# Kernel optimization log

Measured on AMD Instinct MI355X. Metric: run time of the kernel, lower is better.

## Reference

```python
import jax, jax.numpy as jnp
import numpy as np
from jax import lax

B, T = 64, 2048
ENC, DEC, ATT = 512, 1024, 128
NFILT, KSIZE = 32, 31
PAD = KSIZE // 2


def setup_inputs() -> dict:
    key = jax.random.key(0)
    ks = jax.random.split(key, 9)
    query = jax.random.normal(ks[0], (B, 1, DEC), dtype=jnp.float32)
    keys = jax.random.normal(ks[1], (B, T, ENC), dtype=jnp.float32)
    prev_weights = jax.random.uniform(ks[2], (B, T), dtype=jnp.float32)
    mask = jax.random.randint(ks[3], (B, T), 0, 2, dtype=jnp.int32)
    # params stored as [in, out] (transpose of torch Linear weight); same math
    W1 = jax.random.normal(ks[4], (ENC, ATT), dtype=jnp.float32) * (ENC ** -0.5)
    W2 = jax.random.normal(ks[5], (DEC, ATT), dtype=jnp.float32) * (DEC ** -0.5)
    V = jax.random.normal(ks[6], (ATT,), dtype=jnp.float32) * (ATT ** -0.5)
    conv_w = jax.random.normal(ks[7], (NFILT, 1, KSIZE), dtype=jnp.float32) * (KSIZE ** -0.5)
    loc_dense = jax.random.normal(ks[8], (NFILT, ATT), dtype=jnp.float32) * (NFILT ** -0.5)
    return {"query": query, "keys": keys, "prev_weights": prev_weights, "mask": mask,
            "W1": W1, "W2": W2, "V": V, "conv_w": conv_w, "loc_dense": loc_dense}


def reference(query, keys, prev_weights, mask, W1, W2, V, conv_w, loc_dense):
    proj_key = jnp.einsum('bte,ea->bta', keys, W1)          # [B,T,A]
    proj_query = jnp.einsum('bqd,da->bqa', query, W2)       # [B,1,A]
    # location conv: input [B,1,T], kernel [F,1,K], 'same' padding -> [B,F,T]
    loc_feat = lax.conv_general_dilated(prev_weights[:, None, :], conv_w,
                                        window_strides=(1,), padding=[(PAD, PAD)],
                                        dimension_numbers=('NCH', 'OIH', 'NCH'))
    proj_loc = jnp.einsum('bft,fa->bta', loc_feat, loc_dense)  # [B,T,A]
    scores = jnp.einsum('bta,a->bt', jnp.tanh(proj_key + proj_query + proj_loc), V)
    scores = jnp.where(mask == 0, -1e9, scores)
    weights = jax.nn.softmax(scores, axis=-1)                # [B,T]
    context = jnp.einsum('bt,bte->be', weights, keys)[:, None, :]  # [B,1,ENC]
    return context, weights
```

## Files before the change

kernel.cpp:

```cpp
#include <hip/hip_runtime.h>

typedef __attribute__((ext_vector_type(4))) float f32x4;
typedef __attribute__((ext_vector_type(8))) short bf16x8;

#define T_LEN 2048
#define ENC   512
#define DEC   1024
#define ATT   128
#define NB    64
#define NTB   64
#define NSTEP 17

__device__ __forceinline__ unsigned short f2bf_rne(float x) {
  unsigned int u = __builtin_bit_cast(unsigned int, x);
  u += 0x7fff + ((u >> 16) & 1);
  return (unsigned short)(u >> 16);
}
__device__ __forceinline__ short f2bf_fast(float x) {
  unsigned int u = __builtin_bit_cast(unsigned int, x);
  return (short)((u + 0x8000u) >> 16);
}

__device__ __forceinline__ float fast_tanh(float x) {
  float e = __expf(2.f * x);
  return 1.f - 2.f / (e + 1.f);
}

__global__ __launch_bounds__(128) void prep(
    const float* __restrict__ query, const float* __restrict__ W2,
    const float* __restrict__ W1, const float* __restrict__ convw,
    const float* __restrict__ ldense,
    float* __restrict__ pq, unsigned short* __restrict__ Bl) {
  int bidx = blockIdx.x;
  if (bidx < NB) {
    int a = threadIdx.x;
    const float* q = query + bidx * DEC;
    float a0 = 0.f, a1 = 0.f, a2 = 0.f, a3 = 0.f;
    for (int d = 0; d < DEC; d += 4) {
      a0 += q[d]     * W2[(d)     * ATT + a];
      a1 += q[d + 1] * W2[(d + 1) * ATT + a];
      a2 += q[d + 2] * W2[(d + 2) * ATT + a];
      a3 += q[d + 3] * W2[(d + 3) * ATT + a];
    }
    pq[bidx * ATT + a] = (a0 + a1) + (a2 + a3);
  } else {
    int a = bidx - NB;
    int n = a >> 4, rs = a & 15;
    for (int k = threadIdx.x; k < NSTEP * 32; k += 128) {
      float v = 0.f;
      if (k < 512) {
        v = W1[k * ATT + a];
      } else if (k < 543) {
        int kc = k - 512;
        #pragma unroll
        for (int f = 0; f < 32; ++f) v += convw[f * 31 + kc] * ldense[f * ATT + a];
      }
      int t = k >> 5, g = (k & 31) >> 3, j = k & 7;
      Bl[(((t * 8 + n) * 64 + g * 16 + rs) << 3) + j] = f2bf_rne(v);
    }
  }
}

__global__ __launch_bounds__(64, 2) void lsa_main(
    const float* __restrict__ keys, const float* __restrict__ prev,
    const int* __restrict__ mask, const unsigned short* __restrict__ Bl,
    const float* __restrict__ pq, const float* __restrict__ Vv,
    float* __restrict__ wout, float* __restrict__ dpart, float* __restrict__ cpart) {
  __shared__ float e_vals[32];

  const int lane = threadIdx.x;
  const int bid = blockIdx.x;
  const int b = bid >> 6;
  const int row0 = (bid & 63) * 32;
  const int rsel = lane & 15, grp = lane >> 4;

  const float* keyrow = keys + ((size_t)b * T_LEN + row0 + rsel) * ENC + grp * 8;
  const unsigned short* Bp = Bl + lane * 8;

  f32x4 acc[2][8];
  #pragma unroll
  for (int m = 0; m < 2; ++m)
    #pragma unroll
    for (int n = 0; n < 8; ++n) acc[m][n] = (f32x4)0.f;

  f32x4 A0, A1, A2, A3, B0, B1, B2, B3, C0, C1, C2, C3;
  bf16x8 P0, P1, P2, P3, P4, P5, P6, P7;
  bf16x8 Q0, Q1, Q2, Q3, Q4, Q5, Q6, Q7;

#define SB() __builtin_amdgcn_sched_barrier(0)

#define LOADK(S, t_) do { \
    S##0 = *(const f32x4*)(keyrow + (t_) * 32); \
    S##1 = *(const f32x4*)(keyrow + (t_) * 32 + 4); \
    S##2 = *(const f32x4*)(keyrow + 16 * ENC + (t_) * 32); \
    S##3 = *(const f32x4*)(keyrow + 16 * ENC + (t_) * 32 + 4); } while (0)

#define LOADP(S) do { \
    _Pragma("unroll") \
    for (int j_ = 0; j_ < 4; ++j_) { \
      int kk0 = grp * 8 + j_, kk1 = grp * 8 + 4 + j_; \
      int p00 = row0 + rsel + kk0 - 15, p01 = row0 + rsel + kk1 - 15; \
      S##0[j_] = (kk0 < 31 && p00 >= 0 && p00 < T_LEN) ? prev[b * T_LEN + p00] : 0.f; \
      S##1[j_] = (kk1 < 31 && p01 >= 0 && p01 < T_LEN) ? prev[b * T_LEN + p01] : 0.f; \
      S##2[j_] = (kk0 < 31 && p00 + 16 >= 0 && p00 + 16 < T_LEN) ? prev[b * T_LEN + p00 + 16] : 0.f; \
      S##3[j_] = (kk1 < 31 && p01 + 16 >= 0 && p01 + 16 < T_LEN) ? prev[b * T_LEN + p01 + 16] : 0.f; \
    } } while (0)

#define LOADB(S, t_) do { \
    S##0 = *(const bf16x8*)(Bp + ((t_) * 8 + 0) * 512); \
    S##1 = *(const bf16x8*)(Bp + ((t_) * 8 + 1) * 512); \
    S##2 = *(const bf16x8*)(Bp + ((t_) * 8 + 2) * 512); \
    S##3 = *(const bf16x8*)(Bp + ((t_) * 8 + 3) * 512); \
    S##4 = *(const bf16x8*)(Bp + ((t_) * 8 + 4) * 512); \
    S##5 = *(const bf16x8*)(Bp + ((t_) * 8 + 5) * 512); \
    S##6 = *(const bf16x8*)(Bp + ((t_) * 8 + 6) * 512); \
    S##7 = *(const bf16x8*)(Bp + ((t_) * 8 + 7) * 512); } while (0)

#define STEP(S, BB) do { \
    bf16x8 af0, af1; \
    _Pragma("unroll") \
    for (int j_ = 0; j_ < 4; ++j_) { \
      af0[j_] = f2bf_fast(S##0[j_]); af0[4 + j_] = f2bf_fast(S##1[j_]); \
      af1[j_] = f2bf_fast(S##2[j_]); af1[4 + j_] = f2bf_fast(S##3[j_]); \
    } \
    acc[0][0] = __builtin_amdgcn_mfma_f32_16x16x32_bf16(af0, BB##0, acc[0][0], 0, 0, 0); \
    acc[1][0] = __builtin_amdgcn_mfma_f32_16x16x32_bf16(af1, BB##0, acc[1][0], 0, 0, 0); \
    acc[0][1] = __builtin_amdgcn_mfma_f32_16x16x32_bf16(af0, BB##1, acc[0][1], 0, 0, 0); \
    acc[1][1] = __builtin_amdgcn_mfma_f32_16x16x32_bf16(af1, BB##1, acc[1][1], 0, 0, 0); \
    acc[0][2] = __builtin_amdgcn_mfma_f32_16x16x32_bf16(af0, BB##2, acc[0][2], 0, 0, 0); \
    acc[1][2] = __builtin_amdgcn_mfma_f32_16x16x32_bf16(af1, BB##2, acc[1][2], 0, 0, 0); \
    acc[0][3] = __builtin_amdgcn_mfma_f32_16x16x32_bf16(af0, BB##3, acc[0][3], 0, 0, 0); \
    acc[1][3] = __builtin_amdgcn_mfma_f32_16x16x32_bf16(af1, BB##3, acc[1][3], 0, 0, 0); \
    acc[0][4] = __builtin_amdgcn_mfma_f32_16x16x32_bf16(af0, BB##4, acc[0][4], 0, 0, 0); \
    acc[1][4] = __builtin_amdgcn_mfma_f32_16x16x32_bf16(af1, BB##4, acc[1][4], 0, 0, 0); \
    acc[0][5] = __builtin_amdgcn_mfma_f32_16x16x32_bf16(af0, BB##5, acc[0][5], 0, 0, 0); \
    acc[1][5] = __builtin_amdgcn_mfma_f32_16x16x32_bf16(af1, BB##5, acc[1][5], 0, 0, 0); \
    acc[0][6] = __builtin_amdgcn_mfma_f32_16x16x32_bf16(af0, BB##6, acc[0][6], 0, 0, 0); \
    acc[1][6] = __builtin_amdgcn_mfma_f32_16x16x32_bf16(af1, BB##6, acc[1][6], 0, 0, 0); \
    acc[0][7] = __builtin_amdgcn_mfma_f32_16x16x32_bf16(af0, BB##7, acc[0][7], 0, 0, 0); \
    acc[1][7] = __builtin_amdgcn_mfma_f32_16x16x32_bf16(af1, BB##7, acc[1][7], 0, 0, 0); } while (0)

  LOADK(A, 0); LOADK(B, 1); LOADB(P, 0);
  LOADK(C, 2);  LOADB(Q, 1);  SB(); STEP(A, P);
  LOADK(A, 3);  LOADB(P, 2);  SB(); STEP(B, Q);
  LOADK(B, 4);  LOADB(Q, 3);  SB(); STEP(C, P);
  LOADK(C, 5);  LOADB(P, 4);  SB(); STEP(A, Q);
  LOADK(A, 6);  LOADB(Q, 5);  SB(); STEP(B, P);
  LOADK(B, 7);  LOADB(P, 6);  SB(); STEP(C, Q);
  LOADK(C, 8);  LOADB(Q, 7);  SB(); STEP(A, P);
  LOADK(A, 9);  LOADB(P, 8);  SB(); STEP(B, Q);
  LOADK(B, 10); LOADB(Q, 9);  SB(); STEP(C, P);
  LOADK(C, 11); LOADB(P, 10); SB(); STEP(A, Q);
  LOADK(A, 12); LOADB(Q, 11); SB(); STEP(B, P);
  LOADK(B, 13); LOADB(P, 12); SB(); STEP(C, Q);
  LOADK(C, 14); LOADB(Q, 13); SB(); STEP(A, P);
  LOADK(A, 15); LOADB(P, 14); SB(); STEP(B, Q);
  LOADP(B);     LOADB(Q, 15); SB(); STEP(C, P);
  LOADB(P, 16); SB(); STEP(A, Q);
  STEP(B, P);

  float psum[2][4];
  #pragma unroll
  for (int m = 0; m < 2; ++m)
    #pragma unroll
    for (int i = 0; i < 4; ++i) psum[m][i] = 0.f;
  #pragma unroll
  for (int n = 0; n < 8; ++n) {
    int c = n * 16 + rsel;
    float pqv = pq[b * ATT + c];
    float vv = Vv[c];
    #pragma unroll
    for (int m = 0; m < 2; ++m)
      #pragma unroll
      for (int i = 0; i < 4; ++i)
        psum[m][i] += vv * fast_tanh(acc[m][n][i] + pqv);
  }
  #pragma unroll
  for (int m = 0; m < 2; ++m)
    #pragma unroll
    for (int i = 0; i < 4; ++i) {
      float v = psum[m][i];
      v += __shfl_xor(v, 1, 64);
      v += __shfl_xor(v, 2, 64);
      v += __shfl_xor(v, 4, 64);
      v += __shfl_xor(v, 8, 64);
      psum[m][i] = v;
    }
  float esum = 0.f;
  if (rsel == 0) {
    #pragma unroll
    for (int m = 0; m < 2; ++m)
      #pragma unroll
      for (int i = 0; i < 4; ++i) {
        int r = m * 16 + grp * 4 + i;
        int gr = b * T_LEN + row0 + r;
        float e = (mask[gr] == 0) ? 0.f : __expf(psum[m][i]);
        wout[gr] = e;
        e_vals[r] = e;
        esum += e;
      }
  }
  esum += __shfl_xor(esum, 16, 64);
  esum += __shfl_xor(esum, 32, 64);
  if (lane == 0) dpart[bid] = esum;
  __syncthreads();

  {
    const float* kb = keys + ((size_t)b * T_LEN + row0) * ENC + lane * 8;
    f32x4 c0 = (f32x4)0.f, c1 = (f32x4)0.f;
    #pragma unroll
    for (int r = 0; r < 32; ++r) {
      float e = e_vals[r];
      f32x4 k0 = *(const f32x4*)(kb + (size_t)r * ENC);
      f32x4 k1 = *(const f32x4*)(kb + (size_t)r * ENC + 4);
      c0 += e * k0;
      c1 += e * k1;
    }
    *(f32x4*)(cpart + (size_t)bid * ENC + lane * 8) = c0;
    *(f32x4*)(cpart + (size_t)bid * ENC + lane * 8 + 4) = c1;
  }
}

__global__ __launch_bounds__(256) void lsa_finalize(
    const float* __restrict__ dpart, const float* __restrict__ cpart,
    float* __restrict__ out) {
  int b = blockIdx.x, tid = threadIdx.x;
  float d = 0.f;
  #pragma unroll
  for (int i = 0; i < NTB; ++i) d += dpart[b * NTB + i];
  float inv = 1.f / d;
  for (int e = tid; e < ENC; e += 256) {
    float c = 0.f;
    #pragma unroll
    for (int i = 0; i < NTB; ++i) c += cpart[((size_t)(b * NTB + i)) * ENC + e];
    out[b * ENC + e] = c * inv;
  }
  float* wrow = out + NB * ENC + (size_t)b * T_LEN;
  for (int t = tid; t < T_LEN; t += 256) wrow[t] *= inv;
}

extern "C" void kernel_launch(void* const* d_in, const int* in_sizes, int n_in,
                              void* d_out, int out_size, void* d_ws, size_t ws_size,
                              hipStream_t stream) {
  const float* query  = (const float*)d_in[0];
  const float* keys   = (const float*)d_in[1];
  const float* prev   = (const float*)d_in[2];
  const int*   mask   = (const int*)d_in[3];
  const float* W1     = (const float*)d_in[4];
  const float* W2     = (const float*)d_in[5];
  const float* V      = (const float*)d_in[6];
  const float* convw  = (const float*)d_in[7];
  const float* ldense = (const float*)d_in[8];
  float* out = (float*)d_out;

  char* ws = (char*)d_ws;
  unsigned short* Bl = (unsigned short*)ws;
  float* pq    = (float*)(ws + 139264);
  float* dpart = (float*)(ws + 139264 + 32768);
  float* cpart = (float*)(ws + 139264 + 32768 + 16384);

  prep<<<dim3(192), dim3(128), 0, stream>>>(query, W2, W1, convw, ldense, pq, Bl);
  lsa_main<<<dim3(NB * NTB), dim3(64), 0, stream>>>(keys, prev, mask, Bl, pq, V,
                                                    out + NB * ENC, dpart, cpart);
  lsa_finalize<<<dim3(NB), dim3(256), 0, stream>>>(dpart, cpart, out);
}
```

Before: 137.7 us.

## Stage keys and weights through LDS with async global-to-LDS copies

Replaces the direct register loads of key rows and bf16 weight fragments with asynchronous global_load_lds copies into a triple-buffered key area and double-buffered weight area in shared memory. Key rows are laid out with an XOR swizzle to avoid bank conflicts, and explicit vmcnt waits drive the pipeline. Each step then reads its MFMA operands from LDS. This frees vector registers and drops the two-waves-per-SIMD launch bound, but it uses about 37 KB of LDS per 64-thread block, which may limit occupancy, and adds LDS read traffic and hand-tuned wait counts that must stay correct.

After: 136.5 us. Within noise of the previous version (-0.9%).

```diff
diff --git a/kernel.cpp b/kernel.cpp
--- a/kernel.cpp
+++ b/kernel.cpp
@@ -11,6 +11,14 @@
 #define NTB   64
 #define NSTEP 17
 
+typedef unsigned int u32;
+typedef __attribute__((address_space(1))) const u32 gu32;
+typedef __attribute__((address_space(3))) u32 lu32;
+
+__device__ __forceinline__ void async_copy16(const void* g, void* l) {
+  __builtin_amdgcn_global_load_lds((gu32*)g, (lu32*)l, 16, 0, 0);
+}
+
 __device__ __forceinline__ unsigned short f2bf_rne(float x) {
   unsigned int u = __builtin_bit_cast(unsigned int, x);
   u += 0x7fff + ((u >> 16) & 1);
@@ -20,7 +28,6 @@
   unsigned int u = __builtin_bit_cast(unsigned int, x);
   return (short)((u + 0x8000u) >> 16);
 }
-
 __device__ __forceinline__ float fast_tanh(float x) {
   float e = __expf(2.f * x);
   return 1.f - 2.f / (e + 1.f);
@@ -61,21 +68,26 @@
   }
 }
 
-__global__ __launch_bounds__(64, 2) void lsa_main(
+__global__ __launch_bounds__(64) void lsa_main(
     const float* __restrict__ keys, const float* __restrict__ prev,
     const int* __restrict__ mask, const unsigned short* __restrict__ Bl,
     const float* __restrict__ pq, const float* __restrict__ Vv,
     float* __restrict__ wout, float* __restrict__ dpart, float* __restrict__ cpart) {
-  __shared__ float e_vals[32];
+  __shared__ f32x4 SHv[2312];
+  char* SHc = (char*)SHv;
 
   const int lane = threadIdx.x;
   const int bid = blockIdx.x;
   const int b = bid >> 6;
   const int row0 = (bid & 63) * 32;
   const int rsel = lane & 15, grp = lane >> 4;
-
-  const float* keyrow = keys + ((size_t)b * T_LEN + row0 + rsel) * ENC + grp * 8;
-  const unsigned short* Bp = Bl + lane * 8;
+  const int lr = lane >> 3, cp = lane & 7;
+  const int gc = cp ^ lr;
+  const int ca0 = (2 * grp) ^ (rsel & 7);
+  const int ca1 = ca0 ^ 1;
+
+  const float* gAsrc = keys + ((size_t)b * T_LEN + row0 + lr) * ENC + gc * 4;
+  const unsigned short* Bsrc = Bl + lane * 8;
 
   f32x4 acc[2][8];
   #pragma unroll
@@ -83,82 +95,110 @@
     #pragma unroll
     for (int n = 0; n < 8; ++n) acc[m][n] = (f32x4)0.f;
 
-  f32x4 A0, A1, A2, A3, B0, B1, B2, B3, C0, C1, C2, C3;
-  bf16x8 P0, P1, P2, P3, P4, P5, P6, P7;
-  bf16x8 Q0, Q1, Q2, Q3, Q4, Q5, Q6, Q7;
-
-#define SB() __builtin_amdgcn_sched_barrier(0)
-
-#define LOADK(S, t_) do { \
-    S##0 = *(const f32x4*)(keyrow + (t_) * 32); \
-    S##1 = *(const f32x4*)(keyrow + (t_) * 32 + 4); \
-    S##2 = *(const f32x4*)(keyrow + 16 * ENC + (t_) * 32); \
-    S##3 = *(const f32x4*)(keyrow + 16 * ENC + (t_) * 32 + 4); } while (0)
-
-#define LOADP(S) do { \
+#define WAITVM_(n) asm volatile("s_waitcnt vmcnt(" #n ")" ::: "memory")
+#define WAITVM(n) WAITVM_(n)
+#define LGKM0 asm volatile("s_waitcnt lgkmcnt(0)" ::: "memory")
+
+#define STAGE_A(t_, buf_) do { \
+    const float* s_ = gAsrc + (t_) * 32; \
+    char* d_ = SHc + (buf_) * 4096; \
+    async_copy16(s_,            d_); \
+    async_copy16(s_ +  8 * ENC, d_ + 1024); \
+    async_copy16(s_ + 16 * ENC, d_ + 2048); \
+    async_copy16(s_ + 24 * ENC, d_ + 3072); } while (0)
+
+#define STAGE_B(t_, buf_) do { \
+    const unsigned short* s_ = Bsrc + (size_t)(t_) * 4096; \
+    char* d_ = SHc + 12288 + (buf_) * 8192; \
+    _Pragma("unroll") \
+    for (int n_ = 0; n_ < 8; ++n_) \
+      async_copy16(s_ + n_ * 512, d_ + n_ * 1024); } while (0)
+
+#define STAGE_B16() do { \
+    const unsigned short* s_ = Bsrc + (size_t)16 * 4096; \
+    char* d_ = SHc + 28672; \
+    _Pragma("unroll") \
+    for (int n_ = 0; n_ < 8; ++n_) \
+      async_copy16(s_ + n_ * 512, d_ + n_ * 1024); } while (0)
+
+#define KSTEP(ab_, bb_, STAGECODE) do { \
+    const char* Ab_ = SHc + (ab_) * 4096; \
+    const char* Bb_ = SHc + 12288 + (bb_) * 8192; \
+    f32x4 x00 = *(const f32x4*)(Ab_ + rsel * 128 + ca0 * 16); \
+    f32x4 x01 = *(const f32x4*)(Ab_ + rsel * 128 + ca1 * 16); \
+    f32x4 x10 = *(const f32x4*)(Ab_ + (16 + rsel) * 128 + ca0 * 16); \
+    f32x4 x11 = *(const f32x4*)(Ab_ + (16 + rsel) * 128 + ca1 * 16); \
+    bf16x8 bfr[8]; \
+    _Pragma("unroll") \
+    for (int n_ = 0; n_ < 8; ++n_) \
+      bfr[n_] = *(const bf16x8*)(Bb_ + n_ * 1024 + lane * 16); \
+    LGKM0; \
+    STAGECODE; \
+    bf16x8 af0, af1; \
     _Pragma("unroll") \
     for (int j_ = 0; j_ < 4; ++j_) { \
-      int kk0 = grp * 8 + j_, kk1 = grp * 8 + 4 + j_; \
-      int p00 = row0 + rsel + kk0 - 15, p01 = row0 + rsel + kk1 - 15; \
-      S##0[j_] = (kk0 < 31 && p00 >= 0 && p00 < T_LEN) ? prev[b * T_LEN + p00] : 0.f; \
-      S##1[j_] = (kk1 < 31 && p01 >= 0 && p01 < T_LEN) ? prev[b * T_LEN + p01] : 0.f; \
-      S##2[j_] = (kk0 < 31 && p00 + 16 >= 0 && p00 + 16 < T_LEN) ? prev[b * T_LEN + p00 + 16] : 0.f; \
-      S##3[j_] = (kk1 < 31 && p01 + 16 >= 0 && p01 + 16 < T_LEN) ? prev[b * T_LEN + p01 + 16] : 0.f; \
+      af0[j_] = f2bf_fast(x00[j_]); af0[4 + j_] = f2bf_fast(x01[j_]); \
+      af1[j_] = f2bf_fast(x10[j_]); af1[4 + j_] = f2bf_fast(x11[j_]); \
+    } \
+    _Pragma("unroll") \
+    for (int n_ = 0; n_ < 8; ++n_) { \
+      acc[0][n_] = __builtin_amdgcn_mfma_f32_16x16x32_bf16(af0, bfr[n_], acc[0][n_], 0, 0, 0); \
+      acc[1][n_] = __builtin_amdgcn_mfma_f32_16x16x32_bf16(af1, bfr[n_], acc[1][n_], 0, 0, 0); \
     } } while (0)
 
-#define LOADB(S, t_) do { \
-    S##0 = *(const bf16x8*)(Bp + ((t_) * 8 + 0) * 512); \
-    S##1 = *(const bf16x8*)(Bp + ((t_) * 8 + 1) * 512); \
-    S##2 = *(const bf16x8*)(Bp + ((t_) * 8 + 2) * 512); \
-    S##3 = *(const bf16x8*)(Bp + ((t_) * 8 + 3) * 512); \
-    S##4 = *(const bf16x8*)(Bp + ((t_) * 8 + 4) * 512); \
-    S##5 = *(const bf16x8*)(Bp + ((t_) * 8 + 5) * 512); \
-    S##6 = *(const bf16x8*)(Bp + ((t_) * 8 + 6) * 512); \
-    S##7 = *(const bf16x8*)(Bp + ((t_) * 8 + 7) * 512); } while (0)
-
-#define STEP(S, BB) do { \
-    bf16x8 af0, af1; \
-    _Pragma("unroll") \
-    for (int j_ = 0; j_ < 4; ++j_) { \
-      af0[j_] = f2bf_fast(S##0[j_]); af0[4 + j_] = f2bf_fast(S##1[j_]); \
-      af1[j_] = f2bf_fast(S##2[j_]); af1[4 + j_] = f2bf_fast(S##3[j_]); \
-    } \
-    acc[0][0] = __builtin_amdgcn_mfma_f32_16x16x32_bf16(af0, BB##0, acc[0][0], 0, 0, 0); \
-    acc[1][0] = __builtin_amdgcn_mfma_f32_16x16x32_bf16(af1, BB##0, acc[1][0], 0, 0, 0); \
-    acc[0][1] = __builtin_amdgcn_mfma_f32_16x16x32_bf16(af0, BB##1, acc[0][1], 0, 0, 0); \
-    acc[1][1] = __builtin_amdgcn_mfma_f32_16x16x32_bf16(af1, BB##1, acc[1][1], 0, 0, 0); \
-    acc[0][2] = __builtin_amdgcn_mfma_f32_16x16x32_bf16(af0, BB##2, acc[0][2], 0, 0, 0); \
-    acc[1][2] = __builtin_amdgcn_mfma_f32_16x16x32_bf16(af1, BB##2, acc[1][2], 0, 0, 0); \
-    acc[0][3] = __builtin_amdgcn_mfma_f32_16x16x32_bf16(af0, BB##3, acc[0][3], 0, 0, 0); \
-    acc[1][3] = __builtin_amdgcn_mfma_f32_16x16x32_bf16(af1, BB##3, acc[1][3], 0, 0, 0); \
-    acc[0][4] = __builtin_amdgcn_mfma_f32_16x16x32_bf16(af0, BB##4, acc[0][4], 0, 0, 0); \
-    acc[1][4] = __builtin_amdgcn_mfma_f32_16x16x32_bf16(af1, BB##4, acc[1][4], 0, 0, 0); \
-    acc[0][5] = __builtin_amdgcn_mfma_f32_16x16x32_bf16(af0, BB##5, acc[0][5], 0, 0, 0); \
-    acc[1][5] = __builtin_amdgcn_mfma_f32_16x16x32_bf16(af1, BB##5, acc[1][5], 0, 0, 0); \
-    acc[0][6] = __builtin_amdgcn_mfma_f32_16x16x32_bf16(af0, BB##6, acc[0][6], 0, 0, 0); \
-    acc[1][6] = __builtin_amdgcn_mfma_f32_16x16x32_bf16(af1, BB##6, acc[1][6], 0, 0, 0); \
-    acc[0][7] = __builtin_amdgcn_mfma_f32_16x16x32_bf16(af0, BB##7, acc[0][7], 0, 0, 0); \
-    acc[1][7] = __builtin_amdgcn_mfma_f32_16x16x32_bf16(af1, BB##7, acc[1][7], 0, 0, 0); } while (0)
-
-  LOADK(A, 0); LOADK(B, 1); LOADB(P, 0);
-  LOADK(C, 2);  LOADB(Q, 1);  SB(); STEP(A, P);
-  LOADK(A, 3);  LOADB(P, 2);  SB(); STEP(B, Q);
-  LOADK(B, 4);  LOADB(Q, 3);  SB(); STEP(C, P);
-  LOADK(C, 5);  LOADB(P, 4);  SB(); STEP(A, Q);
-  LOADK(A, 6);  LOADB(Q, 5);  SB(); STEP(B, P);
-  LOADK(B, 7);  LOADB(P, 6);  SB(); STEP(C, Q);
-  LOADK(C, 8);  LOADB(Q, 7);  SB(); STEP(A, P);
-  LOADK(A, 9);  LOADB(P, 8);  SB(); STEP(B, Q);
-  LOADK(B, 10); LOADB(Q, 9);  SB(); STEP(C, P);
-  LOADK(C, 11); LOADB(P, 10); SB(); STEP(A, Q);
-  LOADK(A, 12); LOADB(Q, 11); SB(); STEP(B, P);
-  LOADK(B, 13); LOADB(P, 12); SB(); STEP(C, Q);
-  LOADK(C, 14); LOADB(Q, 13); SB(); STEP(A, P);
-  LOADK(A, 15); LOADB(P, 14); SB(); STEP(B, Q);
-  LOADP(B);     LOADB(Q, 15); SB(); STEP(C, P);
-  LOADB(P, 16); SB(); STEP(A, Q);
-  STEP(B, P);
-
+  f32x4 CV0, CV1, CV2, CV3;
+  #pragma unroll
+  for (int j = 0; j < 4; ++j) {
+    int kk0 = grp * 8 + j, kk1 = grp * 8 + 4 + j;
+    int p00 = row0 + rsel + kk0 - 15, p01 = row0 + rsel + kk1 - 15;
+    CV0[j] = (kk0 < 31 && p00 >= 0 && p00 < T_LEN) ? prev[b * T_LEN + p00] : 0.f;
+    CV1[j] = (kk1 < 31 && p01 >= 0 && p01 < T_LEN) ? prev[b * T_LEN + p01] : 0.f;
+    CV2[j] = (kk0 < 31 && p00 + 16 >= 0 && p00 + 16 < T_LEN) ? prev[b * T_LEN + p00 + 16] : 0.f;
+    CV3[j] = (kk1 < 31 && p01 + 16 >= 0 && p01 + 16 < T_LEN) ? prev[b * T_LEN + p01 + 16] : 0.f;
+  }
+
+  STAGE_B(0, 0); STAGE_A(0, 0);
+  STAGE_B(1, 1); STAGE_A(1, 1);
+  STAGE_A(2, 2);
+
+  WAITVM(16); KSTEP(0, 0, { STAGE_B(2, 0);  STAGE_A(3, 0);  });
+  WAITVM(16); KSTEP(1, 1, { STAGE_B(3, 1);  STAGE_A(4, 1);  });
+  WAITVM(16); KSTEP(2, 0, { STAGE_B(4, 0);  STAGE_A(5, 2);  });
+  WAITVM(16); KSTEP(0, 1, { STAGE_B(5, 1);  STAGE_A(6, 0);  });
+  WAITVM(16); KSTEP(1, 0, { STAGE_B(6, 0);  STAGE_A(7, 1);  });
+  WAITVM(16); KSTEP(2, 1, { STAGE_B(7, 1);  STAGE_A(8, 2);  });
+  WAITVM(16); KSTEP(0, 0, { STAGE_B(8, 0);  STAGE_A(9, 0);  });
+  WAITVM(16); KSTEP(1, 1, { STAGE_B(9, 1);  STAGE_A(10, 1); });
+  WAITVM(16); KSTEP(2, 0, { STAGE_B(10, 0); STAGE_A(11, 2); });
+  WAITVM(16); KSTEP(0, 1, { STAGE_B(11, 1); STAGE_A(12, 0); });
+  WAITVM(16); KSTEP(1, 0, { STAGE_B(12, 0); STAGE_A(13, 1); });
+  WAITVM(16); KSTEP(2, 1, { STAGE_B(13, 1); STAGE_A(14, 2); });
+  WAITVM(16); KSTEP(0, 0, { STAGE_B(14, 0); STAGE_A(15, 0); });
+  WAITVM(16); KSTEP(1, 1, { STAGE_B(15, 1); STAGE_B16();    });
+  WAITVM(20); KSTEP(2, 0, { });
+  WAITVM(8);  KSTEP(0, 1, { });
+  {
+    WAITVM(0);
+    const char* Bb = SHc + 28672;
+    bf16x8 bfr[8];
+    #pragma unroll
+    for (int n = 0; n < 8; ++n)
+      bfr[n] = *(const bf16x8*)(Bb + n * 1024 + lane * 16);
+    LGKM0;
+    bf16x8 af0, af1;
+    #pragma unroll
+    for (int j = 0; j < 4; ++j) {
+      af0[j] = f2bf_fast(CV0[j]); af0[4 + j] = f2bf_fast(CV1[j]);
+      af1[j] = f2bf_fast(CV2[j]); af1[4 + j] = f2bf_fast(CV3[j]);
+    }
+    #pragma unroll
+    for (int n = 0; n < 8; ++n) {
+      acc[0][n] = __builtin_amdgcn_mfma_f32_16x16x32_bf16(af0, bfr[n], acc[0][n], 0, 0, 0);
+      acc[1][n] = __builtin_amdgcn_mfma_f32_16x16x32_bf16(af1, bfr[n], acc[1][n], 0, 0, 0);
+    }
+  }
+
+  float* e_vals = (float*)(SHc + 36864);
   float psum[2][4];
   #pragma unroll
   for (int m = 0; m < 2; ++m)
```
